# Optimization experiments

Measured on AMD Instinct MI355X. Metric: run time of the kernel, lower is better.

The kernel has to match this reference:

```python
import jax, jax.numpy as jnp
import numpy as np

B, S, D, H = 2, 4096, 512, 8
DK = D // H  # 64


def setup_inputs() -> dict:
    key = jax.random.key(0)
    ks = jax.random.split(key, 7)
    scale = 1.0 / np.sqrt(D)
    return {
        "query": jax.random.normal(ks[0], (B, S, D), dtype=jnp.float32),
        "key": jax.random.normal(ks[1], (B, S, D), dtype=jnp.float32),
        "value": jax.random.normal(ks[2], (B, S, D), dtype=jnp.float32),
        # nn.Linear weights, stored [out, in] as in torch; y = x @ W.T
        "Wq": jax.random.normal(ks[3], (D, D), dtype=jnp.float32) * scale,
        "Wk": jax.random.normal(ks[4], (D, D), dtype=jnp.float32) * scale,
        "Wv": jax.random.normal(ks[5], (D, D), dtype=jnp.float32) * scale,
        "Wo": jax.random.normal(ks[6], (D, D), dtype=jnp.float32) * scale,
    }


def reference(query, key, value, Wq, Wk, Wv, Wo):
    # projections (torch Linear: x @ W.T)
    q = query @ Wq.T  # [B,S,D]
    k = key @ Wk.T
    v = value @ Wv.T
    # split heads -> [B,H,S,DK]
    q = q.reshape(B, S, H, DK).transpose(0, 2, 1, 3)
    k = k.reshape(B, S, H, DK).transpose(0, 2, 1, 3)
    v = v.reshape(B, S, H, DK).transpose(0, 2, 1, 3)
    # scores [B,H,S,S], softmax, weighted sum (dropout=0 / eval)
    scores = jnp.einsum("bhqd,bhkd->bhqk", q, k) / np.sqrt(DK).astype(np.float32)
    weights = jax.nn.softmax(scores, axis=-1)
    attn = jnp.einsum("bhqk,bhkd->bhqd", weights, v)  # [B,H,S,DK]
    # merge heads -> [B,S,D], output projection
    out = attn.transpose(0, 2, 1, 3).reshape(B, S, D)
    return out @ Wo.T
```

## Files before the change

### kernel.cpp

```cpp
#include <hip/hip_runtime.h>
#include <hip/hip_bf16.h>

typedef short short8 __attribute__((ext_vector_type(8)));
typedef short short4v __attribute__((ext_vector_type(4)));
typedef float floatx4 __attribute__((ext_vector_type(4)));
typedef unsigned int uint4v __attribute__((ext_vector_type(4)));

constexpr int Bc = 2, Sc = 4096, Dc = 512, Hc = 8, DKc = 64;
constexpr int Mc = Bc * Sc;

static __device__ __forceinline__ unsigned short f2bf(float f) {
  unsigned int u = __builtin_bit_cast(unsigned int, f);
  unsigned int rb = ((u >> 16) & 1u) + 0x7fffu;
  return (unsigned short)((u + rb) >> 16);
}
static __device__ __forceinline__ unsigned int cvt_pk_bf16(float lo, float hi) {
  unsigned int r;
  asm("v_cvt_pk_bf16_f32 %0, %1, %2" : "=v"(r) : "v"(lo), "v"(hi));
  return r;
}
static __device__ __forceinline__ float exp2_fast(float x) {
  float r;
  asm("v_exp_f32 %0, %1" : "=v"(r) : "v"(x));
  return r;
}

__global__ __launch_bounds__(256) void cast_w(
    const float* __restrict__ a, const float* __restrict__ b,
    const float* __restrict__ c, const float* __restrict__ d,
    unsigned short* __restrict__ out) {
  const float* srcs[4] = {a, b, c, d};
  const int m = blockIdx.y;
  const int i = (blockIdx.x * 256 + threadIdx.x) * 4;
  float4 v = *(const float4*)(srcs[m] + i);
  unsigned short t4[4] = {f2bf(v.x), f2bf(v.y), f2bf(v.z), f2bf(v.w)};
  *(short4v*)(out + (size_t)m * (Dc * Dc) + i) = *(short4v*)t4;
}

template <int IN_F32, int OUT_F32>
__global__ __launch_bounds__(256) void gemm_bt(
    const void* __restrict__ Xv, const unsigned short* __restrict__ Wb,
    void* __restrict__ Yv, int Mdim, int N, int K) {
  constexpr int BM = 128, BN = 64, BK = 32, LDP = 40;
  __shared__ unsigned short As[BM * LDP];
  __shared__ unsigned short Bs[BN * LDP];
  const int tid = threadIdx.x;
  const int lane = tid & 63, wid = tid >> 6;
  const int wm = wid >> 1, wn = wid & 1;
  const int bm = blockIdx.y * BM, bn = blockIdx.x * BN;
  const int rq = lane & 15, kk8 = (lane >> 4) * 8;
  const int sr = tid >> 1, sc = (tid & 1) * 16;
  const int brow = tid >> 2, bc8 = (tid & 3) * 8;

  floatx4 acc[4][2] = {};

  for (int k0 = 0; k0 < K; k0 += BK) {
    if (IN_F32) {
      const float* src = (const float*)Xv + (size_t)(bm + sr) * K + k0 + sc;
      unsigned int t2[8];
#pragma unroll
      for (int i = 0; i < 4; ++i) {
        float4 v = *(const float4*)(src + i * 4);
        t2[i * 2 + 0] = cvt_pk_bf16(v.x, v.y);
        t2[i * 2 + 1] = cvt_pk_bf16(v.z, v.w);
      }
      uint4v u0 = {t2[0], t2[1], t2[2], t2[3]};
      uint4v u1 = {t2[4], t2[5], t2[6], t2[7]};
      *(uint4v*)&As[sr * LDP + sc] = u0;
      *(uint4v*)&As[sr * LDP + sc + 8] = u1;
    } else {
      const unsigned short* src =
          (const unsigned short*)Xv + (size_t)(bm + sr) * K + k0 + sc;
      *(short8*)&As[sr * LDP + sc] = *(const short8*)src;
      *(short8*)&As[sr * LDP + sc + 8] = *(const short8*)(src + 8);
    }
    *(short8*)&Bs[brow * LDP + bc8] =
        *(const short8*)(Wb + (size_t)(bn + brow) * K + k0 + bc8);
    __syncthreads();

    short8 af[4], bfr[2];
#pragma unroll
    for (int mi = 0; mi < 4; ++mi)
      af[mi] = *(const short8*)&As[(wm * 64 + mi * 16 + rq) * LDP + kk8];
#pragma unroll
    for (int ni = 0; ni < 2; ++ni)
      bfr[ni] = *(const short8*)&Bs[(wn * 32 + ni * 16 + rq) * LDP + kk8];
#pragma unroll
    for (int mi = 0; mi < 4; ++mi)
#pragma unroll
      for (int ni = 0; ni < 2; ++ni)
        acc[mi][ni] = __builtin_amdgcn_mfma_f32_16x16x32_bf16(
            af[mi], bfr[ni], acc[mi][ni], 0, 0, 0);
    __syncthreads();
  }

#pragma unroll
  for (int mi = 0; mi < 4; ++mi)
#pragma unroll
    for (int ni = 0; ni < 2; ++ni)
#pragma unroll
      for (int j = 0; j < 4; ++j) {
        int r = bm + wm * 64 + mi * 16 + (lane >> 4) * 4 + j;
        int c = bn + wn * 32 + ni * 16 + rq;
        float v = acc[mi][ni][j];
        if (OUT_F32)
          ((float*)Yv)[(size_t)r * N + c] = v;
        else
          ((unsigned short*)Yv)[(size_t)r * N + c] = f2bf(v);
      }
}

__global__ __launch_bounds__(256) void transpose_v(
    const unsigned short* __restrict__ vb, unsigned short* __restrict__ vt) {
  constexpr int LDT = 65;
  __shared__ unsigned short T[64 * LDT];
  const int tid = threadIdx.x;
  const int s0 = blockIdx.x * 64, c0 = blockIdx.y * 64, b = blockIdx.z;
  const int r = tid >> 2, cs = (tid & 3) * 16;
  const unsigned short* src = vb + ((size_t)b * Sc + s0 + r) * Dc + c0 + cs;
  *(short8*)&T[r * LDT + cs] = *(const short8*)src;
  *(short8*)&T[r * LDT + cs + 8] = *(const short8*)(src + 8);
  __syncthreads();
  unsigned short* dst = vt + ((size_t)b * Dc + c0 + r) * Sc + s0 + cs;
  unsigned short tmp[16];
#pragma unroll
  for (int j = 0; j < 16; ++j) tmp[j] = T[(cs + j) * LDT + r];
  *(short8*)dst = *(short8*)&tmp[0];
  *(short8*)(dst + 8) = *(short8*)&tmp[8];
}

__global__ __launch_bounds__(512, 4) void attn_fwd(
    const unsigned short* __restrict__ Qp, const unsigned short* __restrict__ Kp,
    const unsigned short* __restrict__ Vtp, unsigned short* __restrict__ Op) {
  __shared__ unsigned char smem[36864];
  unsigned short* Ks = (unsigned short*)smem;
  unsigned short* Vs = (unsigned short*)(smem + 8192);
  unsigned short* PsB = (unsigned short*)(smem + 16384);

  const int tid = threadIdx.x, lane = tid & 63, wid = tid >> 6;
  const int qc = wid >> 1, kh = wid & 1;
  const int b = blockIdx.y >> 3, h = blockIdx.y & 7;
  const int q0 = blockIdx.x * 128 + qc * 32;
  const int rq = lane & 15, lg = lane >> 4, kk8 = lg * 8;

  unsigned short* Psw = PsB + wid * 1280;

  const unsigned short* Qb = Qp + ((size_t)b * Sc) * Dc + h * DKc;
  const unsigned short* Kb = Kp + ((size_t)b * Sc) * Dc + h * DKc;
  const unsigned short* Vh = Vtp + ((size_t)b * Dc + h * DKc) * Sc;

  short8 qa[2][2];
#pragma unroll
  for (int qi = 0; qi < 2; ++qi)
#pragma unroll
    for (int c = 0; c < 2; ++c)
      qa[qi][c] = *(const short8*)(Qb + (size_t)(q0 + qi * 16 + rq) * Dc + c * 32 + kk8);

  floatx4 o_acc[2][4] = {};
  float l_part[2] = {0.f, 0.f};
  float m_run[2] = {-1e30f, -1e30f};

  const float C2 = 0.18033688f;
  const float THR = 8.0f;

  const int sr = tid >> 3, sc8 = (tid & 7) * 8;
  const int st = (sr * 64 + sc8) ^ ((sr & 7) << 3);
  const int sx = (rq & 7) << 3;

  for (int it = 0; it < 64; ++it) {
    const int k0 = it * 64;
    *(short8*)&Ks[st] = *(const short8*)(Kb + (size_t)(k0 + sr) * Dc + sc8);
    *(short8*)&Vs[st] = *(const short8*)(Vh + (size_t)sr * Sc + k0 + sc8);
    __syncthreads();

    short8 ka[2][2];
#pragma unroll
    for (int ks = 0; ks < 2; ++ks)
#pragma unroll
      for (int c = 0; c < 2; ++c) {
        const int row = kh * 32 + ks * 16 + rq;
        ka[ks][c] = *(const short8*)&Ks[(row * 64 + c * 32 + kk8) ^ sx];
      }

#pragma unroll
    for (int qi = 0; qi < 2; ++qi) {
      floatx4 s[2] = {};
#pragma unroll
      for (int ks = 0; ks < 2; ++ks) {
        s[ks] = __builtin_amdgcn_mfma_f32_16x16x32_bf16(ka[ks][0], qa[qi][0], s[ks], 0, 0, 0);
        s[ks] = __builtin_amdgcn_mfma_f32_16x16x32_bf16(ka[ks][1], qa[qi][1], s[ks], 0, 0, 0);
      }
      float tp = fmaxf(fmaxf(fmaxf(s[0][0], s[0][1]), fmaxf(s[0][2], s[0][3])),
                       fmaxf(fmaxf(s[1][0], s[1][1]), fmaxf(s[1][2], s[1][3]))) * C2;

      if (__any(tp > m_run[qi] + THR)) {
        float tm = tp;
        tm = fmaxf(tm, __shfl_xor(tm, 16, 64));
        tm = fmaxf(tm, __shfl_xor(tm, 32, 64));
        if (__any(tm > m_run[qi])) {
          float mn = fmaxf(m_run[qi], tm);
          float scf = exp2_fast(m_run[qi] - mn);
          m_run[qi] = mn;
          l_part[qi] *= scf;
          float sc_c[4];
#pragma unroll
          for (int j = 0; j < 4; ++j) sc_c[j] = __shfl(scf, lg * 4 + j, 64);
#pragma unroll
          for (int j = 0; j < 4; ++j)
#pragma unroll
            for (int dt = 0; dt < 4; ++dt) o_acc[qi][dt][j] *= sc_c[j];
        }
      }

      const float lm = m_run[qi];
#pragma unroll
      for (int ks = 0; ks < 2; ++ks) {
        float p0 = exp2_fast(fmaf(s[ks][0], C2, -lm));
        float p1 = exp2_fast(fmaf(s[ks][1], C2, -lm));
        float p2 = exp2_fast(fmaf(s[ks][2], C2, -lm));
        float p3 = exp2_fast(fmaf(s[ks][3], C2, -lm));
        l_part[qi] += (p0 + p1) + (p2 + p3);
        unsigned long long pv =
            (unsigned long long)cvt_pk_bf16(p0, p1) |
            ((unsigned long long)cvt_pk_bf16(p2, p3) << 32);
        *(unsigned long long*)&Psw[qi * 640 + rq * 40 + ks * 16 + lg * 4] = pv;
      }
    }

    short8 pa0 = *(const short8*)&Psw[0 * 640 + rq * 40 + kk8];
    short8 pa1 = *(const short8*)&Psw[1 * 640 + rq * 40 + kk8];
#pragma unroll
    for (int dt = 0; dt < 4; ++dt) {
      const int vrow = dt * 16 + rq;
      short8 v = *(const short8*)&Vs[(vrow * 64 + kh * 32 + kk8) ^ sx];
      o_acc[0][dt] = __builtin_amdgcn_mfma_f32_16x16x32_bf16(pa0, v, o_acc[0][dt], 0, 0, 0);
      o_acc[1][dt] = __builtin_amdgcn_mfma_f32_16x16x32_bf16(pa1, v, o_acc[1][dt], 0, 0, 0);
    }
    __syncthreads();
  }

  float l_run[2];
#pragma unroll
  for (int qi = 0; qi < 2; ++qi) {
    float ls = l_part[qi];
    ls += __shfl_xor(ls, 16, 64);
    ls += __shfl_xor(ls, 32, 64);
    l_run[qi] = ls;
  }

  float* MO = (float*)smem;
  float* ML = (float*)(smem + 32768);
  if (kh == 1) {
#pragma unroll
    for (int qi = 0; qi < 2; ++qi) {
#pragma unroll
      for (int j = 0; j < 4; ++j) {
        int row = qc * 32 + qi * 16 + lg * 4 + j;
#pragma unroll
        for (int dt = 0; dt < 4; ++dt)
          MO[(size_t)row * 64 + dt * 16 + rq] = o_acc[qi][dt][j];
      }
      if (lg == 0) {
        int row = qc * 32 + qi * 16 + rq;
        ML[row * 2 + 0] = m_run[qi];
        ML[row * 2 + 1] = l_run[qi];
      }
    }
  }
  __syncthreads();
  if (kh == 0) {
#pragma unroll
    for (int qi = 0; qi < 2; ++qi) {
      float m0c[4], l0c[4];
#pragma unroll
      for (int j = 0; j < 4; ++j) {
        m0c[j] = __shfl(m_run[qi], lg * 4 + j, 64);
        l0c[j] = __shfl(l_run[qi], lg * 4 + j, 64);
      }
#pragma unroll
      for (int j = 0; j < 4; ++j) {
        int row = qc * 32 + qi * 16 + lg * 4 + j;
        int r = q0 + qi * 16 + lg * 4 + j;
        float m1 = ML[row * 2 + 0], l1 = ML[row * 2 + 1];
        float mx = fmaxf(m0c[j], m1);
        float a0 = exp2_fast(m0c[j] - mx), a1 = exp2_fast(m1 - mx);
        float inv = 1.0f / (l0c[j] * a0 + l1 * a1);
#pragma unroll
        for (int dt = 0; dt < 4; ++dt) {
          float o = (o_acc[qi][dt][j] * a0 + MO[(size_t)row * 64 + dt * 16 + rq] * a1) * inv;
          Op[((size_t)b * Sc + r) * Dc + h * DKc + dt * 16 + rq] = f2bf(o);
        }
      }
    }
  }
}

extern "C" void kernel_launch(void* const* d_in, const int* in_sizes, int n_in,
                              void* d_out, int out_size, void* d_ws, size_t ws_size,
                              hipStream_t stream) {
  const float* q_in = (const float*)d_in[0];
  const float* k_in = (const float*)d_in[1];
  const float* v_in = (const float*)d_in[2];
  const float* Wq = (const float*)d_in[3];
  const float* Wk = (const float*)d_in[4];
  const float* Wv = (const float*)d_in[5];
  const float* Wo = (const float*)d_in[6];

  unsigned short* wq_b = (unsigned short*)d_ws;
  unsigned short* wk_b = wq_b + Dc * Dc;
  unsigned short* wv_b = wk_b + Dc * Dc;
  unsigned short* wo_b = wv_b + Dc * Dc;
  unsigned short* qb = wo_b + Dc * Dc;
  unsigned short* kb = qb + (size_t)Mc * Dc;
  unsigned short* vb = kb + (size_t)Mc * Dc;
  unsigned short* ab = vb + (size_t)Mc * Dc;
  unsigned short* vt = ab + (size_t)Mc * Dc;

  dim3 cg(Dc * Dc / 4 / 256, 4);
  cast_w<<<cg, 256, 0, stream>>>(Wq, Wk, Wv, Wo, wq_b);

  dim3 gg(Dc / 64, Mc / 128);
  gemm_bt<1, 0><<<gg, 256, 0, stream>>>(q_in, wq_b, qb, Mc, Dc, Dc);
  gemm_bt<1, 0><<<gg, 256, 0, stream>>>(k_in, wk_b, kb, Mc, Dc, Dc);
  gemm_bt<1, 0><<<gg, 256, 0, stream>>>(v_in, wv_b, vb, Mc, Dc, Dc);

  dim3 tg(Sc / 64, Dc / 64, Bc);
  transpose_v<<<tg, 256, 0, stream>>>(vb, vt);

  dim3 ga(Sc / 128, Bc * Hc);
  attn_fwd<<<ga, 512, 0, stream>>>(qb, kb, vt, ab);

  gemm_bt<0, 1><<<gg, 256, 0, stream>>>(ab, wo_b, (float*)d_out, Mc, Dc, Dc);
}
```

Before: 193.9 us.

## Keep softmax P in registers by permuting V key order during transpose

The P tile is no longer written to and read back from per-wave LDS. It is packed straight from the MFMA score accumulators into the A-operand registers for the PV MFMA. To make the register layout match the key order, the V transpose kernel now writes keys in a permuted order within each 32-key group. This removes LDS traffic and waits per iteration and shrinks shared memory use, but it depends on the permutation exactly matching the MFMA lane mapping.

```diff
diff --git a/kernel.cpp b/kernel.cpp
--- a/kernel.cpp
+++ b/kernel.cpp
@@ -121,21 +121,26 @@
   *(short8*)&T[r * LDT + cs] = *(const short8*)src;
   *(short8*)&T[r * LDT + cs + 8] = *(const short8*)(src + 8);
   __syncthreads();
-  unsigned short* dst = vt + ((size_t)b * Dc + c0 + r) * Sc + s0 + cs;
   unsigned short tmp[16];
 #pragma unroll
   for (int j = 0; j < 16; ++j) tmp[j] = T[(cs + j) * LDT + r];
-  *(short8*)dst = *(short8*)&tmp[0];
-  *(short8*)(dst + 8) = *(short8*)&tmp[8];
+  const int k4 = (cs >> 4) & 1;
+  const int base32 = s0 + (cs & 32);
+  unsigned short* dstrow = vt + ((size_t)b * Dc + c0 + r) * Sc;
+#pragma unroll
+  for (int g = 0; g < 4; ++g) {
+    short4v v4 = {(short)tmp[4 * g + 0], (short)tmp[4 * g + 1],
+                  (short)tmp[4 * g + 2], (short)tmp[4 * g + 3]};
+    *(short4v*)(dstrow + base32 + g * 8 + k4 * 4) = v4;
+  }
 }
 
 __global__ __launch_bounds__(512, 4) void attn_fwd(
     const unsigned short* __restrict__ Qp, const unsigned short* __restrict__ Kp,
     const unsigned short* __restrict__ Vtp, unsigned short* __restrict__ Op) {
-  __shared__ unsigned char smem[36864];
+  __shared__ unsigned char smem[33792];
   unsigned short* Ks = (unsigned short*)smem;
   unsigned short* Vs = (unsigned short*)(smem + 8192);
-  unsigned short* PsB = (unsigned short*)(smem + 16384);
 
   const int tid = threadIdx.x, lane = tid & 63, wid = tid >> 6;
   const int qc = wid >> 1, kh = wid & 1;
@@ -143,8 +148,6 @@
   const int q0 = blockIdx.x * 128 + qc * 32;
   const int rq = lane & 15, lg = lane >> 4, kk8 = lg * 8;
 
-  unsigned short* Psw = PsB + wid * 1280;
-
   const unsigned short* Qb = Qp + ((size_t)b * Sc) * Dc + h * DKc;
   const unsigned short* Kb = Kp + ((size_t)b * Sc) * Dc + h * DKc;
   const unsigned short* Vh = Vtp + ((size_t)b * Dc + h * DKc) * Sc;
@@ -182,6 +185,7 @@
         ka[ks][c] = *(const short8*)&Ks[(row * 64 + c * 32 + kk8) ^ sx];
       }
 
+    short8 pb_[2];
 #pragma unroll
     for (int qi = 0; qi < 2; ++qi) {
       floatx4 s[2] = {};
@@ -213,28 +217,35 @@
       }
 
       const float lm = m_run[qi];
-#pragma unroll
-      for (int ks = 0; ks < 2; ++ks) {
-        float p0 = exp2_fast(fmaf(s[ks][0], C2, -lm));
-        float p1 = exp2_fast(fmaf(s[ks][1], C2, -lm));
-        float p2 = exp2_fast(fmaf(s[ks][2], C2, -lm));
-        float p3 = exp2_fast(fmaf(s[ks][3], C2, -lm));
+      unsigned int pw0, pw1, pw2, pw3;
+      {
+        float p0 = exp2_fast(fmaf(s[0][0], C2, -lm));
+        float p1 = exp2_fast(fmaf(s[0][1], C2, -lm));
+        float p2 = exp2_fast(fmaf(s[0][2], C2, -lm));
+        float p3 = exp2_fast(fmaf(s[0][3], C2, -lm));
         l_part[qi] += (p0 + p1) + (p2 + p3);
-        unsigned long long pv =
-            (unsigned long long)cvt_pk_bf16(p0, p1) |
-            ((unsigned long long)cvt_pk_bf16(p2, p3) << 32);
-        *(unsigned long long*)&Psw[qi * 640 + rq * 40 + ks * 16 + lg * 4] = pv;
-      }
-    }
-
-    short8 pa0 = *(const short8*)&Psw[0 * 640 + rq * 40 + kk8];
-    short8 pa1 = *(const short8*)&Psw[1 * 640 + rq * 40 + kk8];
+        pw0 = cvt_pk_bf16(p0, p1);
+        pw1 = cvt_pk_bf16(p2, p3);
+      }
+      {
+        float p0 = exp2_fast(fmaf(s[1][0], C2, -lm));
+        float p1 = exp2_fast(fmaf(s[1][1], C2, -lm));
+        float p2 = exp2_fast(fmaf(s[1][2], C2, -lm));
+        float p3 = exp2_fast(fmaf(s[1][3], C2, -lm));
+        l_part[qi] += (p0 + p1) + (p2 + p3);
+        pw2 = cvt_pk_bf16(p0, p1);
+        pw3 = cvt_pk_bf16(p2, p3);
+      }
+      uint4v pw = {pw0, pw1, pw2, pw3};
+      pb_[qi] = __builtin_bit_cast(short8, pw);
+    }
+
 #pragma unroll
     for (int dt = 0; dt < 4; ++dt) {
       const int vrow = dt * 16 + rq;
       short8 v = *(const short8*)&Vs[(vrow * 64 + kh * 32 + kk8) ^ sx];
-      o_acc[0][dt] = __builtin_amdgcn_mfma_f32_16x16x32_bf16(pa0, v, o_acc[0][dt], 0, 0, 0);
-      o_acc[1][dt] = __builtin_amdgcn_mfma_f32_16x16x32_bf16(pa1, v, o_acc[1][dt], 0, 0, 0);
+      o_acc[0][dt] = __builtin_amdgcn_mfma_f32_16x16x32_bf16(pb_[0], v, o_acc[0][dt], 0, 0, 0);
+      o_acc[1][dt] = __builtin_amdgcn_mfma_f32_16x16x32_bf16(pb_[1], v, o_acc[1][dt], 0, 0, 0);
     }
     __syncthreads();
   }
```

Result: faster. 186.4 us (-3.9%).
